# Kernel optimization log

Measured on AMD Instinct MI355X. Metric: run time of the kernel, lower is better.

The kernel has to match this reference:

```python
import jax, jax.numpy as jnp
import numpy as np

# dims
B, K, DIN, PROJ = 32, 256, 512, 64
DM, NL, PL, ST = 128, 3, 8, 4
NPAT = (K - PL) // ST + 1          # 63 patches
DI = 2 * DM                        # mamba inner dim = 256
D_STATE, D_CONV, DT_RANK = 16, 4, 8

def rmsnorm(x, w):
    return x * jax.lax.rsqrt(jnp.mean(x * x, -1, keepdims=True) + 1e-5) * w

def setup_inputs() -> dict:
    key = jax.random.key(0)
    ks = jax.random.split(key, 20)
    s = 0.02
    n = lambda k, sh: (jax.random.normal(k, sh, jnp.float32) * s)
    inp = {
        'x': jax.random.normal(ks[0], (B, K, DIN), jnp.float32),
        'W_proj': n(ks[1], (DIN, PROJ)), 'b_proj': jnp.zeros((PROJ,), jnp.float32),
        'W_embed': n(ks[2], (PL, DM)), 'b_embed': jnp.zeros((DM,), jnp.float32),
        'norm_w': jnp.ones((NL, DM), jnp.float32),
        'in_proj_w': n(ks[3], (NL, DM, 2 * DI)),
        'conv_w': n(ks[4], (NL, DI, 1, D_CONV)), 'conv_b': jnp.zeros((NL, DI), jnp.float32),
        'x_proj_w': n(ks[5], (NL, DI, DT_RANK + 2 * D_STATE)),
        'dt_proj_w': n(ks[6], (NL, DT_RANK, DI)),
        'dt_proj_b': jnp.full((NL, DI), -4.0, jnp.float32),  # softplus -> small dt
        'A_log': jnp.broadcast_to(jnp.log(jnp.arange(1, D_STATE + 1, dtype=jnp.float32)), (NL, DI, D_STATE)).copy(),
        'Dp': jnp.ones((NL, DI), jnp.float32),
        'out_proj_w': n(ks[7], (NL, DI, DM)),
        'final_norm_w': jnp.ones((DM,), jnp.float32),
        'head_flat_w': n(ks[8], (NPAT * DM, 1)), 'head_flat_b': jnp.zeros((1,), jnp.float32),
        'W_head': n(ks[9], (PROJ, 2)), 'b_head': jnp.zeros((2,), jnp.float32),
    }
    return inp

def _mamba(u, Wi, cw, cb, Wx, Wdt, bdt, A_log, Dp, Wo):
    # u: (N, L, DM)
    xz = u @ Wi                                   # (N, L, 2*DI)
    xh, z = jnp.split(xz, 2, axis=-1)
    # causal depthwise conv1d
    xc = jnp.pad(xh.transpose(0, 2, 1), ((0, 0), (0, 0), (D_CONV - 1, 0)))
    xc = jax.lax.conv_general_dilated(xc, cw, (1,), 'VALID',
                                      feature_group_count=DI,
                                      dimension_numbers=('NCH', 'OIH', 'NCH'))
    xh = jax.nn.silu(xc.transpose(0, 2, 1) + cb)  # (N, L, DI)
    dbl = xh @ Wx
    dt = dbl[..., :DT_RANK]
    Bm = dbl[..., DT_RANK:DT_RANK + D_STATE]
    Cm = dbl[..., DT_RANK + D_STATE:]
    delta = jax.nn.softplus(dt @ Wdt + bdt)       # (N, L, DI)
    A = -jnp.exp(A_log)                           # (DI, D_STATE)

    def step(h, t):
        d_t, b_t, c_t, u_t = t                    # (N,DI),(N,S),(N,S),(N,DI)
        h = h * jnp.exp(d_t[..., None] * A) + (d_t * u_t)[..., None] * b_t[:, None, :]
        return h, jnp.einsum('nds,ns->nd', h, c_t)

    h0 = jnp.zeros((u.shape[0], DI, D_STATE), u.dtype)
    xs = (delta.transpose(1, 0, 2), Bm.transpose(1, 0, 2),
          Cm.transpose(1, 0, 2), xh.transpose(1, 0, 2))
    _, ys = jax.lax.scan(step, h0, xs)            # (L, N, DI)
    y = ys.transpose(1, 0, 2) + xh * Dp
    y = y * jax.nn.silu(z)
    return y @ Wo

def reference(x, W_proj, b_proj, W_embed, b_embed, norm_w, in_proj_w, conv_w, conv_b,
              x_proj_w, dt_proj_w, dt_proj_b, A_log, Dp, out_proj_w,
              final_norm_w, head_flat_w, head_flat_b, W_head, b_head):
    h = x @ W_proj + b_proj                       # (B, K, PROJ)
    h = h.transpose(0, 2, 1)                      # (B, C, K)
    idx = np.arange(NPAT)[:, None] * ST + np.arange(PL)[None, :]
    p = h[..., idx]                               # (B, C, NPAT, PL)
    u = p @ W_embed + b_embed                     # (B, C, NPAT, DM)
    u = u.reshape(B * PROJ, NPAT, DM)
    for l in range(NL):
        u = u + _mamba(rmsnorm(u, norm_w[l]), in_proj_w[l], conv_w[l], conv_b[l],
                       x_proj_w[l], dt_proj_w[l], dt_proj_b[l], A_log[l], Dp[l], out_proj_w[l])
    u = rmsnorm(u, final_norm_w)
    u = u.reshape(B, PROJ, NPAT * DM)
    y = (u @ head_flat_w + head_flat_b)[..., 0]   # (B, C)
    return y @ W_head + b_head                    # (B, 2)
```

## Files before the change

kernel.cpp:

```cpp
#include <hip/hip_runtime.h>
#include <hip/hip_bf16.h>
#include <cstdio>

typedef __hip_bfloat16 bf16;
typedef __attribute__((ext_vector_type(8))) short short8;
typedef __attribute__((ext_vector_type(4))) short short4v;
typedef __attribute__((ext_vector_type(4))) float f32x4;
typedef __attribute__((ext_vector_type(2))) float f32x2;

#define NB    32
#define NK    256
#define NDIN  512
#define NPROJ 64
#define NDM   128
#define NNL   3
#define NT    63
#define NDI   256
#define NSEQ  2048
#define NROW  (NSEQ*NT)
#define LDP   136

static __device__ __forceinline__ float b2f(bf16 v){ return __bfloat162float(v); }
static __device__ __forceinline__ bf16  f2b(float v){ return __float2bfloat16(v); }
static __device__ __forceinline__ unsigned short f2bs(float v){
  unsigned int u = __float_as_uint(v);
  return (unsigned short)((u + 0x7FFFu + ((u >> 16) & 1u)) >> 16);
}
static __device__ __forceinline__ float bs2f(unsigned short b){
  return __uint_as_float(((unsigned int)b) << 16);
}
static __device__ __forceinline__ f32x2 lo2(f32x4 v){ f32x2 r; r.x = v.x; r.y = v.y; return r; }
static __device__ __forceinline__ f32x2 hi2(f32x4 v){ f32x2 r; r.x = v.z; r.y = v.w; return r; }
static __device__ __forceinline__ float siluf(float x){
  return x * __builtin_amdgcn_rcpf(1.f + __expf(-x));
}
static __device__ __forceinline__ float softplusf(float x){
  float e = __expf(-fabsf(x));
  return fmaxf(x, 0.f) + __logf(1.f + e);
}

__global__ __launch_bounds__(256) void k_tw_all(
    const float* __restrict__ Wi, const float* __restrict__ Wo,
    const float* __restrict__ Wx,
    unsigned short* __restrict__ WiT, unsigned short* __restrict__ WoT,
    unsigned short* __restrict__ WxT)
{
  int bx = blockIdx.x;
  int l = bx / 704, r = bx - l*704;
  const float* src; unsigned short* dst; int K, srcN, nvalid, n;
  if (r < 512)      { n = r;     src = Wi + (size_t)l*128*512; dst = WiT + (size_t)l*512*128; K=128; srcN=512; nvalid=512; }
  else if (r < 640) { n = r-512; src = Wo + (size_t)l*256*128; dst = WoT + (size_t)l*128*256; K=256; srcN=128; nvalid=128; }
  else              { n = r-640; src = Wx + (size_t)l*256*40;  dst = WxT + (size_t)l*64*256;  K=256; srcN=40;  nvalid=40; }
  for (int k = threadIdx.x; k < K; k += 256) {
    float v = (n < nvalid) ? src[(size_t)k*srcN + n] : 0.f;
    dst[(size_t)n*K + k] = f2bs(v);
  }
}

__global__ __launch_bounds__(64) void k_proj(const float* __restrict__ x,
                       const float* __restrict__ Wp,
                       const float* __restrict__ bp, float* __restrict__ hp)
{
  int b  = blockIdx.x >> 6;
  int kq = blockIdx.x & 63;
  __shared__ float xr[4][NDIN+1];
  for (int e = threadIdx.x; e < 4*NDIN; e += 64) {
    int row = e >> 9, col = e & 511;
    xr[row][col] = x[(size_t)(b*NK + kq*4 + row)*NDIN + col];
  }
  __syncthreads();
  int p = threadIdx.x;
  float bias = bp[p];
  float a0 = bias, a1 = bias, a2 = bias, a3 = bias;
  #pragma unroll 4
  for (int d = 0; d < NDIN; ++d) {
    float w = Wp[d*NPROJ + p];
    a0 += xr[0][d]*w; a1 += xr[1][d]*w; a2 += xr[2][d]*w; a3 += xr[3][d]*w;
  }
  float* dst = hp + (size_t)(b*NPROJ + p)*NK + kq*4;
  dst[0] = a0; dst[1] = a1; dst[2] = a2; dst[3] = a3;
}

__global__ __launch_bounds__(256, 4) void k_embed(const float* __restrict__ hp,
                        const float* __restrict__ We,
                        const float* __restrict__ be, unsigned short* __restrict__ u)
{
  __shared__ float sWe[8][NDM];
  __shared__ float sbe[NDM];
  for (int e = threadIdx.x; e < 8*NDM; e += 256) sWe[e >> 7][e & 127] = We[e];
  if (threadIdx.x < NDM) sbe[threadIdx.x] = be[threadIdx.x];
  __syncthreads();
  int r = blockIdx.x*64 + (threadIdx.x >> 2);
  int strip = (threadIdx.x & 3) * 32;
  int n = r / NT, t = r - n*NT;
  const float* hr = hp + (size_t)n*NK + t*4;
  float h[8];
  #pragma unroll
  for (int j = 0; j < 8; ++j) h[j] = hr[j];
  float acc[32];
  #pragma unroll
  for (int c = 0; c < 32; ++c) acc[c] = sbe[strip + c];
  #pragma unroll
  for (int j = 0; j < 8; ++j)
    #pragma unroll
    for (int c = 0; c < 32; ++c)
      acc[c] += h[j] * sWe[j][strip + c];
  unsigned short* dst = u + (size_t)r*NDM + strip;
  #pragma unroll
  for (int g = 0; g < 4; ++g) {
    short8 o;
    #pragma unroll
    for (int i = 0; i < 8; ++i) o[i] = (short)f2bs(acc[g*8 + i]);
    *(short8*)&dst[g*8] = o;
  }
}

__global__ __launch_bounds__(256) void k_inproj(
    const unsigned short* __restrict__ ub, const unsigned short* __restrict__ WT,
    unsigned short* __restrict__ xh, unsigned short* __restrict__ zb,
    const float* __restrict__ nw)
{
  __shared__ short As[64*LDP];
  __shared__ short Bs[128*LDP];
  const int tid  = threadIdx.x;
  const int r0   = blockIdx.x * 64;
  const int w    = tid >> 6;
  const int lane = tid & 63;
  const int l16  = lane & 15;
  const int quad = lane >> 4;
  const int WM   = (w >> 1) * 32;
  const int WN   = (w & 1) * 64;

  #pragma unroll
  for (int j = 0; j < 4; ++j) {
    int c = tid + j*256;
    int row = c >> 4, k8 = (c & 15) << 3;
    short8 vb = *(const short8*)&ub[(size_t)(r0+row)*128 + k8];
    float f[8];
    #pragma unroll
    for (int i = 0; i < 8; ++i) f[i] = bs2f((unsigned short)vb[i]);
    float ss = 0.f;
    #pragma unroll
    for (int i = 0; i < 8; ++i) ss += f[i]*f[i];
    #pragma unroll
    for (int m = 8; m >= 1; m >>= 1) ss += __shfl_xor(ss, m, 16);
    float sc = rsqrtf(ss*(1.f/128.f) + 1e-5f);
    const float4 nw0 = *(const float4*)&nw[k8];
    const float4 nw1 = *(const float4*)&nw[k8+4];
    short8 o;
    o[0] = (short)f2bs(f[0]*sc*nw0.x); o[1] = (short)f2bs(f[1]*sc*nw0.y);
    o[2] = (short)f2bs(f[2]*sc*nw0.z); o[3] = (short)f2bs(f[3]*sc*nw0.w);
    o[4] = (short)f2bs(f[4]*sc*nw1.x); o[5] = (short)f2bs(f[5]*sc*nw1.y);
    o[6] = (short)f2bs(f[6]*sc*nw1.z); o[7] = (short)f2bs(f[7]*sc*nw1.w);
    *(short8*)&As[row*LDP + k8] = o;
  }

  for (int ny = 0; ny < 4; ++ny) {
    if (ny) __syncthreads();
    #pragma unroll
    for (int j = 0; j < 8; ++j) {
      int c = tid + j*256;
      int n = c >> 4, k8 = (c & 15) << 3;
      *(short8*)&Bs[n*LDP + k8] =
          *(const short8*)&WT[(size_t)(ny*128 + n)*128 + k8];
    }
    __syncthreads();

    f32x4 acc[2][4] = {};
    #pragma unroll
    for (int ks = 0; ks < 4; ++ks) {
      short8 a[2], b[4];
      #pragma unroll
      for (int i = 0; i < 2; ++i)
        a[i] = *(const short8*)&As[(WM + i*16 + l16)*LDP + ks*32 + quad*8];
      #pragma unroll
      for (int j = 0; j < 4; ++j)
        b[j] = *(const short8*)&Bs[(WN + j*16 + l16)*LDP + ks*32 + quad*8];
      #pragma unroll
      for (int i = 0; i < 2; ++i)
        #pragma unroll
        for (int j = 0; j < 4; ++j)
          acc[i][j] = __builtin_amdgcn_mfma_f32_16x16x32_bf16(a[i], b[j], acc[i][j], 0, 0, 0);
    }
    #pragma unroll
    for (int i = 0; i < 2; ++i) {
      #pragma unroll
      for (int j = 0; j < 4; ++j) {
        #pragma unroll
        for (int rr = 0; rr < 4; ++rr) {
          int row = r0 + WM + i*16 + quad*4 + rr;
          int col = ny*128 + WN + j*16 + l16;
          float v = acc[i][j][rr];
          if (col < 256) xh[(size_t)row*256 + col]       = f2bs(v);
          else           zb[(size_t)row*256 + col - 256] = f2bs(siluf(v));
        }
      }
    }
  }
}

template<int MODE, int KTOT, int BN>
__global__ __launch_bounds__(256) void
k_mgemm(const void* __restrict__ Aptr, const unsigned short* __restrict__ WT,
        void* __restrict__ Cptr)
{
  constexpr int MJ = BN/32;
  __shared__ short As[64*LDP];
  __shared__ short Bs[BN*LDP];

  const int tid  = threadIdx.x;
  const int r0   = blockIdx.x * 64;
  const int w    = tid >> 6;
  const int lane = tid & 63;
  const int l16  = lane & 15;
  const int quad = lane >> 4;
  const int WM   = (w >> 1) * 32;
  const int WN   = (w & 1) * (BN/2);

  f32x4 acc[2][MJ] = {};

  for (int kc = 0; kc < KTOT; kc += 128) {
    #pragma unroll
    for (int j = 0; j < 4; ++j) {
      int c   = tid + j*256;
      int row = c >> 4, k8 = (c & 15) << 3;
      short8 v = *(const short8*)((const unsigned short*)Aptr
                                  + (size_t)(r0+row)*256 + kc + k8);
      *(short8*)&As[row*LDP + k8] = v;
    }
    #pragma unroll
    for (int j = 0; j < BN/16; ++j) {
      int c  = tid + j*256;
      int n  = c >> 4, k8 = (c & 15) << 3;
      short8 v = *(const short8*)(WT + (size_t)n*KTOT + kc + k8);
      *(short8*)&Bs[n*LDP + k8] = v;
    }
    __syncthreads();

    #pragma unroll
    for (int ks = 0; ks < 4; ++ks) {
      short8 a[2], b[MJ];
      #pragma unroll
      for (int i = 0; i < 2; ++i)
        a[i] = *(const short8*)&As[(WM + i*16 + l16)*LDP + ks*32 + quad*8];
      #pragma unroll
      for (int j = 0; j < MJ; ++j)
        b[j] = *(const short8*)&Bs[(WN + j*16 + l16)*LDP + ks*32 + quad*8];
      #pragma unroll
      for (int i = 0; i < 2; ++i)
        #pragma unroll
        for (int j = 0; j < MJ; ++j)
          acc[i][j] = __builtin_amdgcn_mfma_f32_16x16x32_bf16(a[i], b[j], acc[i][j], 0, 0, 0);
    }
    __syncthreads();
  }

  #pragma unroll
  for (int i = 0; i < 2; ++i) {
    #pragma unroll
    for (int j = 0; j < MJ; ++j) {
      #pragma unroll
      for (int rr = 0; rr < 4; ++rr) {
        int row = r0 + WM + i*16 + quad*4 + rr;
        int col = WN + j*16 + l16;
        float v = acc[i][j][rr];
        if (MODE == 1) {
          if (col < 40) ((float*)Cptr)[(size_t)row*40 + col] = v;
        } else {
          unsigned short* p = (unsigned short*)Cptr + (size_t)row*128 + col;
          *p = f2bs(bs2f(*p) + v);
        }
      }
    }
  }
}

__global__ __launch_bounds__(256, 8) void k_conv(bf16* __restrict__ xh,
                       const float* __restrict__ cw, const float* __restrict__ cb)
{
  int n = blockIdx.x, d = threadIdx.x;
  float w0 = cw[d*4+0], w1 = cw[d*4+1];
  float w2 = cw[d*4+2], w3 = cw[d*4+3];
  float bias = cb[d];
  float xm3 = 0.f, xm2 = 0.f, xm1 = 0.f;
  bf16* ptr = xh + (size_t)n*NT*256 + d;
  for (int t = 0; t < NT; ++t) {
    float xt = b2f(ptr[0]);
    float a  = bias + w0*xm3 + w1*xm2 + w2*xm1 + w3*xt;
    ptr[0] = f2b(siluf(a));
    ptr += 256;
    xm3 = xm2; xm2 = xm1; xm1 = xt;
  }
}

__global__ __launch_bounds__(128, 4) void k_scan(const float* __restrict__ dbl,
                       const bf16* __restrict__ z, bf16* __restrict__ xh,
                       const float* __restrict__ Wdt, const float* __restrict__ bdt,
                       const float* __restrict__ Alog, const float* __restrict__ Dpp)
{
  int n = blockIdx.x;
  int tid = threadIdx.x;
  int lane = tid & 63, wv = tid >> 6;
  __shared__ __align__(16) float sd[NT+1][40];
  for (int i = tid; i < NT*40; i += 128)
    sd[i/40][i%40] = dbl[(size_t)n*NT*40 + i];
  if (tid < 40) sd[NT][tid] = 0.f;
  __syncthreads();

  const int dbase = lane + 128*wv;
  float bd[2], dp2[2];
  f32x2 wdt2[2][4];
  bool chain = true;
  #pragma unroll
  for (int j = 0; j < 2; ++j) {
    int d = dbase + 64*j;
    bd[j]  = bdt[d];
    dp2[j] = Dpp[d];
    #pragma unroll
    for (int r = 0; r < 4; ++r) {
      f32x2 wv2; wv2.x = Wdt[(2*r)*256 + d]; wv2.y = Wdt[(2*r+1)*256 + d];
      wdt2[j][r] = wv2;
    }
    float a0 = -__expf(Alog[d*16]);
    chain = chain && (fabsf(a0 + 1.f) <= 1e-3f);
    #pragma unroll
    for (int s = 1; s < 16; ++s) {
      float as = -__expf(Alog[d*16 + s]);
      chain = chain && (fabsf(as - (float)(s+1)*a0) <= 1e-3f*(float)(s+1));
    }
  }

  const unsigned short* zp = (const unsigned short*)z + (size_t)n*NT*256 + dbase;
  unsigned short*       up = (unsigned short*)xh + (size_t)n*NT*256 + dbase;

  if (chain) {
    f32x2 h2[2][8];
    #pragma unroll
    for (int j = 0; j < 2; ++j)
      #pragma unroll
      for (int s = 0; s < 8; ++s) { h2[j][s].x = 0.f; h2[j][s].y = 0.f; }

    float us[2], zs[2];
    #pragma unroll
    for (int j = 0; j < 2; ++j) { us[j] = bs2f(up[64*j]); zs[j] = bs2f(zp[64*j]); }
    f32x4 dA = *(const f32x4*)&sd[0][0];
    f32x4 dB = *(const f32x4*)&sd[0][4];

    for (int t = 0; t < NT; ++t) {
      const f32x4 Bv0 = *(const f32x4*)&sd[t][8];
      const f32x4 Bv1 = *(const f32x4*)&sd[t][12];
      const f32x4 Bv2 = *(const f32x4*)&sd[t][16];
      const f32x4 Bv3 = *(const f32x4*)&sd[t][20];
      const f32x4 Cv0 = *(const f32x4*)&sd[t][24];
      const f32x4 Cv1 = *(const f32x4*)&sd[t][28];
      const f32x4 Cv2 = *(const f32x4*)&sd[t][32];
      const f32x4 Cv3 = *(const f32x4*)&sd[t][36];
      const f32x4 dAn = *(const f32x4*)&sd[t+1][0];
      const f32x4 dBn = *(const f32x4*)&sd[t+1][4];
      float un[2], zn[2];
      #pragma unroll
      for (int j = 0; j < 2; ++j) { un[j] = bs2f(up[256 + 64*j]); zn[j] = bs2f(zp[256 + 64*j]); }

      #pragma unroll
      for (int j = 0; j < 2; ++j) {
        f32x2 a2; a2.x = bd[j]; a2.y = 0.f;
        a2 += lo2(dA)*wdt2[j][0];
        a2 += hi2(dA)*wdt2[j][1];
        a2 += lo2(dB)*wdt2[j][2];
        a2 += hi2(dB)*wdt2[j][3];
        float dtv = a2.x + a2.y;
        float q  = __expf(-fabsf(dtv));
        float r1 = __builtin_amdgcn_rcpf(1.f + q);
        float E  = dtv > 0.f ? q*r1 : r1;
        float delta = fmaxf(dtv, 0.f) - __logf(r1);
        float E2v = E*E;
        f32x2 ee; ee.x = E2v; ee.y = E2v;
        f32x2 pcur; pcur.x = E; pcur.y = E2v;
        float du = delta*us[j];
        f32x2 du2; du2.x = du; du2.y = du;
        f32x2 y2; y2.x = 0.f; y2.y = 0.f;

        h2[j][0] = h2[j][0]*pcur + du2*lo2(Bv0);  y2 += h2[j][0]*lo2(Cv0);  pcur = pcur*ee;
        h2[j][1] = h2[j][1]*pcur + du2*hi2(Bv0);  y2 += h2[j][1]*hi2(Cv0);  pcur = pcur*ee;
        h2[j][2] = h2[j][2]*pcur + du2*lo2(Bv1);  y2 += h2[j][2]*lo2(Cv1);  pcur = pcur*ee;
        h2[j][3] = h2[j][3]*pcur + du2*hi2(Bv1);  y2 += h2[j][3]*hi2(Cv1);  pcur = pcur*ee;
        h2[j][4] = h2[j][4]*pcur + du2*lo2(Bv2);  y2 += h2[j][4]*lo2(Cv2);  pcur = pcur*ee;
        h2[j][5] = h2[j][5]*pcur + du2*hi2(Bv2);  y2 += h2[j][5]*hi2(Cv2);  pcur = pcur*ee;
        h2[j][6] = h2[j][6]*pcur + du2*lo2(Bv3);  y2 += h2[j][6]*lo2(Cv3);  pcur = pcur*ee;
        h2[j][7] = h2[j][7]*pcur + du2*hi2(Bv3);  y2 += h2[j][7]*hi2(Cv3);

        float yt = y2.x + y2.y;
        float yv = (yt + us[j]*dp2[j]) * zs[j];
        up[64*j] = f2bs(yv);
      }
      up += 256; zp += 256;
      dA = dAn; dB = dBn;
      us[0] = un[0]; us[1] = un[1]; zs[0] = zn[0]; zs[1] = zn[1];
    }
  } else {
    for (int j = 0; j < 2; ++j) {
      int d = dbase + 64*j;
      float wdt[8];
      #pragma unroll
      for (int r = 0; r < 8; ++r) wdt[r] = Wdt[r*256 + d];
      float Av[16];
      #pragma unroll
      for (int s = 0; s < 16; ++s) Av[s] = -__expf(Alog[d*16 + s]);
      float h[16];
      #pragma unroll
      for (int s = 0; s < 16; ++s) h[s] = 0.f;
      const unsigned short* zq = (const unsigned short*)z + (size_t)n*NT*256 + d;
      unsigned short*       uq = (unsigned short*)xh + (size_t)n*NT*256 + d;
      for (int t = 0; t < NT; ++t) {
        float dtv = bd[j];
        #pragma unroll
        for (int r = 0; r < 8; ++r) dtv += sd[t][r]*wdt[r];
        float delta = softplusf(dtv);
        float ut = bs2f(uq[0]);
        float du = delta*ut;
        float yt = 0.f;
        #pragma unroll
        for (int s = 0; s < 16; ++s) {
          float e = __expf(delta*Av[s]);
          h[s] = h[s]*e + du*sd[t][8+s];
          yt  += h[s]*sd[t][24+s];
        }
        float y = (yt + ut*dp2[j]) * bs2f(zq[0]);
        uq[0] = f2bs(y);
        uq += 256; zq += 256;
      }
    }
  }
}

__global__ __launch_bounds__(256) void k_head(const unsigned short* __restrict__ u,
                       const float* __restrict__ fnw,
                       const float* __restrict__ hw, const float* __restrict__ hfb,
                       float* __restrict__ y1)
{
  int n = blockIdx.x;
  int w = threadIdx.x >> 6, lane = threadIdx.x & 63;
  const float2 fw = *(const float2*)&fnw[lane*2];
  float acc = 0.f;
  for (int t = w; t < NT; t += 4) {
    const ushort2 vb = *(const ushort2*)&u[((size_t)n*NT + t)*NDM + lane*2];
    float vx = bs2f(vb.x), vy = bs2f(vb.y);
    const float2 hv = *(const float2*)&hw[t*NDM + lane*2];
    float ss = vx*vx + vy*vy;
    #pragma unroll
    for (int o = 32; o >= 1; o >>= 1) ss += __shfl_xor(ss, o);
    float sc = rsqrtf(ss*(1.f/128.f) + 1e-5f);
    acc += (vx*fw.x*hv.x + vy*fw.y*hv.y)*sc;
  }
  #pragma unroll
  for (int o = 32; o >= 1; o >>= 1) acc += __shfl_xor(acc, o);
  __shared__ float ws[4];
  if (lane == 0) ws[w] = acc;
  __syncthreads();
  if (threadIdx.x == 0) y1[n] = ws[0] + ws[1] + ws[2] + ws[3] + hfb[0];
}

__global__ __launch_bounds__(64) void k_final(const float* __restrict__ y1,
                        const float* __restrict__ Wh,
                        const float* __restrict__ bh, float* __restrict__ out)
{
  int t = threadIdx.x;
  int b = t >> 1, c = t & 1;
  float acc = bh[c];
  #pragma unroll 8
  for (int p = 0; p < 64; ++p) acc += y1[b*64 + p]*Wh[p*2 + c];
  out[b*2 + c] = acc;
}

extern "C" void kernel_launch(void* const* d_in, const int* in_sizes, int n_in,
                              void* d_out, int out_size, void* d_ws, size_t ws_size,
                              hipStream_t stream)
{
  const float* x    = (const float*)d_in[0];
  const float* Wp   = (const float*)d_in[1];
  const float* bp   = (const float*)d_in[2];
  const float* We   = (const float*)d_in[3];
  const float* be   = (const float*)d_in[4];
  const float* nrm  = (const float*)d_in[5];
  const float* Wi   = (const float*)d_in[6];
  const float* cw   = (const float*)d_in[7];
  const float* cb   = (const float*)d_in[8];
  const float* Wx   = (const float*)d_in[9];
  const float* Wdt  = (const float*)d_in[10];
  const float* bdt  = (const float*)d_in[11];
  const float* Alog = (const float*)d_in[12];
  const float* Dpp  = (const float*)d_in[13];
  const float* Wo   = (const float*)d_in[14];
  const float* fnw  = (const float*)d_in[15];
  const float* hw   = (const float*)d_in[16];
  const float* hfb  = (const float*)d_in[17];
  const float* Wh   = (const float*)d_in[18];
  const float* bh   = (const float*)d_in[19];

  const size_t wt_per_l = (size_t)512*128 + 128*256 + 64*256;
  const size_t fixed_b = (size_t)NROW*NDM*2 + (size_t)NSEQ*NK*4 + NSEQ*4
                       + wt_per_l*2*NNL + 16384;
  const size_t per_seq = (size_t)NT*256*2*2 + (size_t)NT*40*4;
  int ch_seq = NSEQ;
  while (ch_seq > 128 && fixed_b + (size_t)ch_seq*per_seq + 4096 > ws_size)
    ch_seq >>= 1;
  const int nchunk  = NSEQ / ch_seq;
  const int ch_rows = ch_seq * NT;
  fprintf(stderr, "[mamba] ws_size=%zu ch_seq=%d nchunk=%d\n", ws_size, ch_seq, nchunk);

  char* pw = (char*)d_ws;
  unsigned short* u = (unsigned short*)pw; pw += (size_t)NROW*NDM*2;
  float* hp   = (float*)pw; pw += (size_t)NSEQ*NK*4;
  float* y1   = (float*)pw; pw += (size_t)NSEQ*4;
  unsigned short* WiT = (unsigned short*)pw; pw += (size_t)NNL*512*128*2;
  unsigned short* WoT = (unsigned short*)pw; pw += (size_t)NNL*128*256*2;
  unsigned short* WxT = (unsigned short*)pw; pw += (size_t)NNL*64*256*2;
  float* dbl  = (float*)pw; pw += (size_t)ch_rows*40*4;
  bf16*  xh   = (bf16*)pw;  pw += (size_t)ch_rows*256*2 + 1024;
  bf16*  z    = (bf16*)pw;  pw += (size_t)ch_rows*256*2 + 1024;

  k_tw_all<<<3*704, 256, 0, stream>>>(Wi, Wo, Wx, WiT, WoT, WxT);
  k_proj <<<NB*64,   64, 0, stream>>>(x, Wp, bp, hp);
  k_embed<<<NROW/64, 256, 0, stream>>>(hp, We, be, u);

  for (int l = 0; l < NNL; ++l) {
    const float* nw_l  = nrm  + (size_t)l*NDM;
    const float* cw_l  = cw   + (size_t)l*NDI*4;
    const float* cb_l  = cb   + (size_t)l*NDI;
    const float* Wdt_l = Wdt  + (size_t)l*8*NDI;
    const float* bdt_l = bdt  + (size_t)l*NDI;
    const float* Al_l  = Alog + (size_t)l*NDI*16;
    const float* Dp_l  = Dpp  + (size_t)l*NDI;
    const unsigned short* WiT_l = WiT + (size_t)l*512*128;
    const unsigned short* WoT_l = WoT + (size_t)l*128*256;
    const unsigned short* WxT_l = WxT + (size_t)l*64*256;

    for (int c = 0; c < nchunk; ++c) {
      unsigned short* u_c = u + (size_t)c*ch_rows*NDM;
      k_inproj<<<ch_rows/64, 256, 0, stream>>>(
          u_c, WiT_l, (unsigned short*)xh, (unsigned short*)z, nw_l);
      k_conv<<<ch_seq, 256, 0, stream>>>(xh, cw_l, cb_l);
      k_mgemm<1,256,64><<<ch_rows/64, 256, 0, stream>>>(xh, WxT_l, dbl);
      k_scan<<<ch_seq, 128, 0, stream>>>(dbl, z, xh, Wdt_l, bdt_l, Al_l, Dp_l);
      k_mgemm<2,256,128><<<ch_rows/64, 256, 0, stream>>>(xh, WoT_l, u_c);
    }
  }

  k_head <<<NSEQ, 256, 0, stream>>>(u, fnw, hw, hfb, y1);
  k_final<<<1, 64, 0, stream>>>(y1, Wh, bh, (float*)d_out);
}
```

Measured before the change: 712.9 us.

## Replace scalar input projection with bf16 MFMA tiled GEMM

```diff
diff --git a/kernel.cpp b/kernel.cpp
--- a/kernel.cpp
+++ b/kernel.cpp
@@ -41,11 +41,17 @@
 
 __global__ __launch_bounds__(256) void k_tw_all(
     const float* __restrict__ Wi, const float* __restrict__ Wo,
-    const float* __restrict__ Wx,
+    const float* __restrict__ Wx, const float* __restrict__ Wp,
     unsigned short* __restrict__ WiT, unsigned short* __restrict__ WoT,
-    unsigned short* __restrict__ WxT)
+    unsigned short* __restrict__ WxT, unsigned short* __restrict__ WpT)
 {
   int bx = blockIdx.x;
+  if (bx >= 3*704) {
+    int n = bx - 3*704;
+    for (int k = threadIdx.x; k < 512; k += 256)
+      WpT[(size_t)n*512 + k] = f2bs(Wp[(size_t)k*64 + n]);
+    return;
+  }
   int l = bx / 704, r = bx - l*704;
   const float* src; unsigned short* dst; int K, srcN, nvalid, n;
   if (r < 512)      { n = r;     src = Wi + (size_t)l*128*512; dst = WiT + (size_t)l*512*128; K=128; srcN=512; nvalid=512; }
@@ -57,28 +63,73 @@
   }
 }
 
-__global__ __launch_bounds__(64) void k_proj(const float* __restrict__ x,
-                       const float* __restrict__ Wp,
-                       const float* __restrict__ bp, float* __restrict__ hp)
-{
-  int b  = blockIdx.x >> 6;
-  int kq = blockIdx.x & 63;
-  __shared__ float xr[4][NDIN+1];
-  for (int e = threadIdx.x; e < 4*NDIN; e += 64) {
-    int row = e >> 9, col = e & 511;
-    xr[row][col] = x[(size_t)(b*NK + kq*4 + row)*NDIN + col];
-  }
-  __syncthreads();
-  int p = threadIdx.x;
-  float bias = bp[p];
-  float a0 = bias, a1 = bias, a2 = bias, a3 = bias;
-  #pragma unroll 4
-  for (int d = 0; d < NDIN; ++d) {
-    float w = Wp[d*NPROJ + p];
-    a0 += xr[0][d]*w; a1 += xr[1][d]*w; a2 += xr[2][d]*w; a3 += xr[3][d]*w;
-  }
-  float* dst = hp + (size_t)(b*NPROJ + p)*NK + kq*4;
-  dst[0] = a0; dst[1] = a1; dst[2] = a2; dst[3] = a3;
+__global__ __launch_bounds__(256) void k_projm(
+    const float* __restrict__ x, const unsigned short* __restrict__ WpT,
+    const float* __restrict__ bp, float* __restrict__ hp)
+{
+  __shared__ short As[64*LDP];
+  __shared__ short Bs[64*LDP];
+  const int tid = threadIdx.x;
+  const int b   = blockIdx.x >> 2;
+  const int kq  = blockIdx.x & 3;
+  const int r0  = b*NK + kq*64;
+  const int w    = tid >> 6;
+  const int lane = tid & 63;
+  const int l16  = lane & 15;
+  const int quad = lane >> 4;
+  const int WM   = (w >> 1) * 32;
+  const int WN   = (w & 1) * 32;
+
+  f32x4 acc[2][2] = {};
+  for (int kc = 0; kc < 512; kc += 128) {
+    if (kc) __syncthreads();
+    #pragma unroll
+    for (int j = 0; j < 4; ++j) {
+      int c = tid + j*256;
+      int row = c >> 4, k8 = (c & 15) << 3;
+      const float* src = x + (size_t)(r0+row)*512 + kc + k8;
+      float4 v0 = *(const float4*)src;
+      float4 v1 = *(const float4*)(src + 4);
+      short8 o;
+      o[0]=(short)f2bs(v0.x); o[1]=(short)f2bs(v0.y); o[2]=(short)f2bs(v0.z); o[3]=(short)f2bs(v0.w);
+      o[4]=(short)f2bs(v1.x); o[5]=(short)f2bs(v1.y); o[6]=(short)f2bs(v1.z); o[7]=(short)f2bs(v1.w);
+      *(short8*)&As[row*LDP + k8] = o;
+    }
+    #pragma unroll
+    for (int j = 0; j < 4; ++j) {
+      int c = tid + j*256;
+      int n = c >> 4, k8 = (c & 15) << 3;
+      *(short8*)&Bs[n*LDP + k8] = *(const short8*)&WpT[(size_t)n*512 + kc + k8];
+    }
+    __syncthreads();
+    #pragma unroll
+    for (int ks = 0; ks < 4; ++ks) {
+      short8 a[2], bb[2];
+      #pragma unroll
+      for (int i = 0; i < 2; ++i)
+        a[i] = *(const short8*)&As[(WM + i*16 + l16)*LDP + ks*32 + quad*8];
+      #pragma unroll
+      for (int j = 0; j < 2; ++j)
+        bb[j] = *(const short8*)&Bs[(WN + j*16 + l16)*LDP + ks*32 + quad*8];
+      #pragma unroll
+      for (int i = 0; i < 2; ++i)
+        #pragma unroll
+        for (int j = 0; j < 2; ++j)
+          acc[i][j] = __builtin_amdgcn_mfma_f32_16x16x32_bf16(a[i], bb[j], acc[i][j], 0, 0, 0);
+    }
+  }
+  #pragma unroll
+  for (int j = 0; j < 2; ++j) {
+    int col = WN + j*16 + l16;
+    float bias = bp[col];
+    #pragma unroll
+    for (int i = 0; i < 2; ++i) {
+      float4 o;
+      o.x = acc[i][j][0] + bias; o.y = acc[i][j][1] + bias;
+      o.z = acc[i][j][2] + bias; o.w = acc[i][j][3] + bias;
+      *(float4*)&hp[(size_t)(b*64 + col)*256 + kq*64 + WM + i*16 + quad*4] = o;
+    }
+  }
 }
 
 __global__ __launch_bounds__(256, 4) void k_embed(const float* __restrict__ hp,
@@ -499,7 +550,7 @@
 
   const size_t wt_per_l = (size_t)512*128 + 128*256 + 64*256;
   const size_t fixed_b = (size_t)NROW*NDM*2 + (size_t)NSEQ*NK*4 + NSEQ*4
-                       + wt_per_l*2*NNL + 16384;
+                       + wt_per_l*2*NNL + 64*512*2 + 16384;
   const size_t per_seq = (size_t)NT*256*2*2 + (size_t)NT*40*4;
   int ch_seq = NSEQ;
   while (ch_seq > 128 && fixed_b + (size_t)ch_seq*per_seq + 4096 > ws_size)
@@ -515,12 +566,13 @@
   unsigned short* WiT = (unsigned short*)pw; pw += (size_t)NNL*512*128*2;
   unsigned short* WoT = (unsigned short*)pw; pw += (size_t)NNL*128*256*2;
   unsigned short* WxT = (unsigned short*)pw; pw += (size_t)NNL*64*256*2;
+  unsigned short* WpT = (unsigned short*)pw; pw += (size_t)64*512*2;
   float* dbl  = (float*)pw; pw += (size_t)ch_rows*40*4;
   bf16*  xh   = (bf16*)pw;  pw += (size_t)ch_rows*256*2 + 1024;
   bf16*  z    = (bf16*)pw;  pw += (size_t)ch_rows*256*2 + 1024;
 
-  k_tw_all<<<3*704, 256, 0, stream>>>(Wi, Wo, Wx, WiT, WoT, WxT);
-  k_proj <<<NB*64,   64, 0, stream>>>(x, Wp, bp, hp);
+  k_tw_all<<<3*704 + 64, 256, 0, stream>>>(Wi, Wo, Wx, Wp, WiT, WoT, WxT, WpT);
+  k_projm<<<NB*4,   256, 0, stream>>>(x, WpT, bp, hp);
   k_embed<<<NROW/64, 256, 0, stream>>>(hp, We, be, u);
 
   for (int l = 0; l < NNL; ++l) {
```

New measurement: 681.3 us. 4.4% less time.
